# Optimization experiments

Hardware: AMD Instinct MI355X
Metric: run time of the kernel (lower is better)

## Reference

```python
import jax, jax.numpy as jnp
import numpy as np

B, N, IN_FT, OUT_FT = 2, 4096, 512, 256
NEG = -9e15
EPS = 1e-12

def _prelu(x, a):
    return jnp.where(x >= 0, x, a * x)

def _normalize(x):
    n = jnp.sqrt(jnp.sum(x * x, axis=-1, keepdims=True))
    return x / jnp.maximum(n, EPS)

def _xavier(key, shape):
    fan_out, fan_in = shape
    lim = np.sqrt(6.0 / (fan_in + fan_out))
    return jax.random.uniform(key, shape, jnp.float32, -lim, lim)

def setup_inputs() -> dict:
    key = jax.random.key(0)
    ks = jax.random.split(key, 8)
    seq = jax.random.normal(ks[0], (B, N, IN_FT), jnp.float32)
    # sparse-ish random adjacency with self loops, row-normalized (typical GCN input)
    u = jax.random.uniform(ks[1], (B, N, N))
    mask = (u < 0.01).astype(jnp.float32)
    eye = jnp.eye(N, dtype=jnp.float32)[None]
    mask = jnp.maximum(mask, eye)
    adj = mask / jnp.sum(mask, axis=-1, keepdims=True)
    return {
        "seq": seq,
        "adj": adj,
        "W_fc": _xavier(ks[2], (OUT_FT, IN_FT)),
        "W_q": _xavier(ks[3], (OUT_FT, OUT_FT)),
        "W_k": _xavier(ks[4], (OUT_FT, OUT_FT)),
        "W_v1": _xavier(ks[5], (OUT_FT, OUT_FT)),
        "W_v2": _xavier(ks[6], (OUT_FT, OUT_FT)),
        "a_v": jnp.asarray(0.25, jnp.float32),    # PReLU inside to_v
        "a_act": jnp.asarray(0.25, jnp.float32),  # final PReLU self.act
        "bias": jnp.zeros((OUT_FT,), jnp.float32),
    }

def reference(seq, adj, W_fc, W_q, W_k, W_v1, W_v2, a_v, a_act, bias):
    # attn=True, training=False (dropout is identity) path of GCN.forward
    seq_fts = jnp.einsum('bnd,od->bno', seq, W_fc)            # fc (no bias)
    out = jnp.einsum('bmn,bno->bmo', adj, seq_fts)            # bmm(adj, seq_fts)
    out_q = _normalize(jnp.einsum('bno,po->bnp', out, W_q))
    out_k = _normalize(jnp.einsum('bno,po->bnp', out, W_k))
    attn_mx = jax.lax.stop_gradient(jnp.einsum('bmd,bnd->bmn', out_q, out_k))
    div_loss = jnp.mean(jnp.sum((out_q - out_k) ** 2, axis=-1))
    scores = jnp.where(adj > 0, attn_mx, NEG)
    attention = jax.nn.softmax(scores, axis=-1)               # dropout skipped (eval)
    ctx = jnp.einsum('bmn,bno->bmo', attention, out)
    h = _prelu(jnp.einsum('bno,po->bnp', ctx, W_v1), a_v)
    v = jnp.einsum('bno,po->bnp', h, W_v2)
    y = _prelu(v + bias, a_act)
    return (y, div_loss)
```

## Files before the change

kernel.cpp:

```cpp
#include <hip/hip_runtime.h>
#include <hip/hip_bf16.h>


#define NN    4096
#define ROWS  8192
#define OFT   256
#define CAP   128
#define NBLK  512
#define RPB   16
#define EPSN  1e-12f
#define MFMA(a,b,c) __builtin_amdgcn_mfma_f32_16x16x32_bf16((a),(b),(c),0,0,0)

typedef unsigned short ushort_t;
typedef __attribute__((ext_vector_type(8))) short bf16x8;
typedef __attribute__((ext_vector_type(4))) float f32x4;

#define WP_FC   0
#define WP_Q    (16384 * 8)
#define WP_K    (WP_Q + 8192 * 8)
#define WP_V1   (WP_K + 8192 * 8)
#define WP_V2   (WP_V1 + 8192 * 8)

__device__ __forceinline__ float lo_f(unsigned u) { union { unsigned i; float f; } c; c.i = u << 16;          return c.f; }
__device__ __forceinline__ float hi_f(unsigned u) { union { unsigned i; float f; } c; c.i = u & 0xFFFF0000u;  return c.f; }
__device__ __forceinline__ float bf2f(ushort_t u) { union { unsigned i; float f; } c; c.i = (unsigned)u << 16; return c.f; }
__device__ __forceinline__ ushort_t f2bf(float f) {
    union { float f; unsigned i; } c; c.f = f;
    unsigned r = c.i + 0x7FFFu + ((c.i >> 16) & 1u);
    return (ushort_t)(r >> 16);
}
__device__ __forceinline__ unsigned pack2(float a, float b) {
    return (unsigned)f2bf(a) | ((unsigned)f2bf(b) << 16);
}

__device__ __forceinline__ int detect32(const unsigned* w, int tid, int* scnt)
{
    if (tid == 0) *scnt = 0;
    __syncthreads();
    if (tid < 256) {
        union { unsigned i; float f; } c; c.i = w[tid];
        float a = fabsf(c.f);
        if (a > 1e-4f && a < 0.5f) atomicAdd(scnt, 1);
    }
    __syncthreads();
    return *scnt >= 128;
}

__global__ __launch_bounds__(256) void k0_prep(
    const void* __restrict__ Wfc, const void* __restrict__ Wq,
    const void* __restrict__ Wk,  const void* __restrict__ Wv1,
    const void* __restrict__ Wv2, ushort_t* __restrict__ Wp)
{
    __shared__ int scnt;
    const int tid = threadIdx.x;
    const int is32 = detect32((const unsigned*)Wfc, tid, &scnt);
    int sid = blockIdx.x * 256 + tid;
    const void* src; int K, local; ushort_t* dst;
    if (sid < 16384) { src = Wfc; K = 512; local = sid; dst = Wp + WP_FC + (size_t)local * 8; }
    else {
        int s = sid - 16384, which = s >> 13; local = s & 8191;
        const void* ws4[4] = {Wq, Wk, Wv1, Wv2};
        src = ws4[which]; K = 256;
        dst = Wp + WP_Q + (size_t)which * 65536 + (size_t)local * 8;
    }
    int col = local & 255, k8c = local >> 8;
    if (is32) {
        const float* p = (const float*)src + (size_t)col * K + k8c * 8;
        float4 x0 = *(const float4*)p, x1 = *(const float4*)(p + 4);
        uint4 o; o.x = pack2(x0.x, x0.y); o.y = pack2(x0.z, x0.w);
        o.z = pack2(x1.x, x1.y); o.w = pack2(x1.z, x1.w);
        *(uint4*)dst = o;
    } else {
        *(bf16x8*)dst = *(const bf16x8*)((const ushort_t*)src + (size_t)col * K + k8c * 8);
    }
}

__global__ __launch_bounds__(512) void k1_extract_fc(
    const void* __restrict__ seq, const void* __restrict__ adj,
    const void* __restrict__ Wfc, const ushort_t* __restrict__ Wp,
    ushort_t* __restrict__ regA, unsigned* __restrict__ gcv,
    int* __restrict__ cnt)
{
    __shared__ ushort_t Astage[64 * 17 * 8];
    __shared__ unsigned csr_cv[RPB * CAP];
    __shared__ int      csr_n[RPB];
    __shared__ int      scnt;

    const int tid = threadIdx.x, wave = tid >> 6, lane = tid & 63;
    const int t16 = lane & 15, kq = lane >> 4;
    const int b = blockIdx.x, r0 = b * RPB;

    const int is32 = detect32((const unsigned*)Wfc, tid, &scnt);

    for (int rr = 0; rr < 2; ++rr) {
        const int rl = wave * 2 + rr;
        const size_t grow = (size_t)(r0 + rl);
        int cntL = 0, incl, total;
        if (is32) {
            const float4* rowp = (const float4*)((const float*)adj + grow * NN);
            float4 v[16];
#pragma unroll
            for (int t = 0; t < 16; ++t) v[t] = rowp[t * 64 + lane];
#pragma unroll
            for (int t = 0; t < 16; ++t) {
                cntL += (v[t].x > 0.f) + (v[t].y > 0.f) + (v[t].z > 0.f) + (v[t].w > 0.f);
            }
            incl = cntL;
#pragma unroll
            for (int off = 1; off < 64; off <<= 1) {
                int y = __shfl_up(incl, off, 64);
                if (lane >= off) incl += y;
            }
            total = __shfl(incl, 63, 64);
            int p = incl - cntL;
#pragma unroll
            for (int t = 0; t < 16; ++t) {
                float f[4] = {v[t].x, v[t].y, v[t].z, v[t].w};
#pragma unroll
                for (int j = 0; j < 4; ++j)
                    if (f[j] > 0.f) {
                        if (p < CAP) {
                            unsigned col = (t * 64 + lane) * 4 + j;
                            csr_cv[rl * CAP + p] = (col << 16) | f2bf(f[j]);
                        }
                        ++p;
                    }
            }
        } else {
            const uint2* rowp = (const uint2*)((const ushort_t*)adj + grow * NN);
            uint2 v[16];
#pragma unroll
            for (int t = 0; t < 16; ++t) v[t] = rowp[t * 64 + lane];
#pragma unroll
            for (int t = 0; t < 16; ++t) {
                cntL += (lo_f(v[t].x) > 0.f) + (hi_f(v[t].x) > 0.f)
                      + (lo_f(v[t].y) > 0.f) + (hi_f(v[t].y) > 0.f);
            }
            incl = cntL;
#pragma unroll
            for (int off = 1; off < 64; off <<= 1) {
                int y = __shfl_up(incl, off, 64);
                if (lane >= off) incl += y;
            }
            total = __shfl(incl, 63, 64);
            int p = incl - cntL;
#pragma unroll
            for (int t = 0; t < 16; ++t) {
                ushort_t raw[4] = {(ushort_t)(v[t].x & 0xFFFF), (ushort_t)(v[t].x >> 16),
                                   (ushort_t)(v[t].y & 0xFFFF), (ushort_t)(v[t].y >> 16)};
#pragma unroll
                for (int j = 0; j < 4; ++j)
                    if (bf2f(raw[j]) > 0.f) {
                        if (p < CAP) {
                            unsigned col = (t * 64 + lane) * 4 + j;
                            csr_cv[rl * CAP + p] = (col << 16) | raw[j];
                        }
                        ++p;
                    }
            }
        }
        if (lane == 0) csr_n[rl] = (total < CAP) ? total : CAP;
    }
    __syncthreads();
    for (int i = tid; i < RPB * CAP; i += 512)
        gcv[b * (RPB * CAP) + i] = csr_cv[i];
    if (tid < RPB) cnt[r0 + tid] = csr_n[tid];

    {
        int row = tid >> 5, seg = tid & 31;
        bf16x8 f0, f1;
        if (is32) {
            const float* p = (const float*)seq + (size_t)(r0 + row) * 512 + seg * 16;
            float4 x0 = *(const float4*)p, x1 = *(const float4*)(p + 4);
            float4 x2 = *(const float4*)(p + 8), x3 = *(const float4*)(p + 12);
            uint4 a, bq;
            a.x = pack2(x0.x, x0.y); a.y = pack2(x0.z, x0.w);
            a.z = pack2(x1.x, x1.y); a.w = pack2(x1.z, x1.w);
            bq.x = pack2(x2.x, x2.y); bq.y = pack2(x2.z, x2.w);
            bq.z = pack2(x3.x, x3.y); bq.w = pack2(x3.z, x3.w);
            f0 = *(bf16x8*)&a; f1 = *(bf16x8*)&bq;
        } else {
            const ushort_t* p = (const ushort_t*)seq + (size_t)(r0 + row) * 512 + seg * 16;
            f0 = *(const bf16x8*)p; f1 = *(const bf16x8*)(p + 8);
        }
        *(bf16x8*)(Astage + ((seg * 2)     * 17 + row) * 8) = f0;
        *(bf16x8*)(Astage + ((seg * 2 + 1) * 17 + row) * 8) = f1;
    }
    __syncthreads();
    {
        const int col0 = wave * 32 + t16, col1 = col0 + 16;
        const ushort_t* Wm = Wp + WP_FC;
        f32x4 a0 = {0.f,0.f,0.f,0.f}, a1 = {0.f,0.f,0.f,0.f};
        for (int bch = 0; bch < 4; ++bch) {
            bf16x8 wb0[4], wb1[4];
#pragma unroll
            for (int c2 = 0; c2 < 4; ++c2) {
                int k8c = (bch * 4 + c2) * 4 + kq;
                wb0[c2] = *(const bf16x8*)(Wm + ((size_t)k8c * 256 + col0) * 8);
                wb1[c2] = *(const bf16x8*)(Wm + ((size_t)k8c * 256 + col1) * 8);
            }
#pragma unroll
            for (int c2 = 0; c2 < 4; ++c2) {
                int c = bch * 4 + c2;
                bf16x8 af = *(const bf16x8*)(Astage + ((c * 4 + kq) * 17 + t16) * 8);
                a0 = MFMA(af, wb0[c2], a0);
                a1 = MFMA(af, wb1[c2], a1);
            }
        }
#pragma unroll
        for (int r = 0; r < 4; ++r) {
            size_t row = (size_t)(r0 + kq * 4 + r);
            regA[row * OFT + col0] = f2bf(a0[r]);
            regA[row * OFT + col1] = f2bf(a1[r]);
        }
    }
}

__global__ __launch_bounds__(512) void k2_spmm_qk(
    const ushort_t* __restrict__ regA, ushort_t* __restrict__ regC,
    ushort_t* __restrict__ regK, ushort_t* __restrict__ regQ,
    const ushort_t* __restrict__ Wp, const unsigned* __restrict__ gcv,
    const int* __restrict__ cnt, float* __restrict__ part)
{
    __shared__ ushort_t Astage[32 * 17 * 8];
    __shared__ unsigned csr_cv[RPB * CAP];
    __shared__ ushort_t qn_l[RPB * OFT];
    __shared__ float    red[2][RPB][4];
    __shared__ float    dlred[8];

    const int tid = threadIdx.x, wave = tid >> 6, lane = tid & 63;
    const int t16 = lane & 15, kq = lane >> 4;
    const int b = blockIdx.x, r0 = b * RPB;
    const size_t batb = (size_t)(b >> 8) * 4096;

    for (int i = tid; i < RPB * CAP; i += 512)
        csr_cv[i] = gcv[b * (RPB * CAP) + i];
    __syncthreads();

    {
        const int rA = wave * 2, rB = rA + 1;
        const int nA = cnt[r0 + rA], nB = cnt[r0 + rB];
        const int nm = max(nA, nB);
        const ushort_t* gA = regA + batb * OFT;
        float a0[4] = {0,0,0,0}, a1[4] = {0,0,0,0};
        for (int i = 0; i < nm; ++i) {
            if (i < nA) {
                unsigned cv = csr_cv[rA*CAP + i];
                float vvf = bf2f((ushort_t)(cv & 0xFFFF));
                uint2 u = *(const uint2*)(gA + (size_t)(cv >> 16) * OFT + lane * 4);
                a0[0]+=vvf*lo_f(u.x); a0[1]+=vvf*hi_f(u.x); a0[2]+=vvf*lo_f(u.y); a0[3]+=vvf*hi_f(u.y);
            }
            if (i < nB) {
                unsigned cv = csr_cv[rB*CAP + i];
                float vvf = bf2f((ushort_t)(cv & 0xFFFF));
                uint2 u = *(const uint2*)(gA + (size_t)(cv >> 16) * OFT + lane * 4);
                a1[0]+=vvf*lo_f(u.x); a1[1]+=vvf*hi_f(u.x); a1[2]+=vvf*lo_f(u.y); a1[3]+=vvf*hi_f(u.y);
            }
        }
        uint2 s0; s0.x = pack2(a0[0], a0[1]); s0.y = pack2(a0[2], a0[3]);
        uint2 s1; s1.x = pack2(a1[0], a1[1]); s1.y = pack2(a1[2], a1[3]);
        *(uint2*)(regC + (size_t)(r0 + rA) * OFT + lane * 4) = s0;
        *(uint2*)(regC + (size_t)(r0 + rB) * OFT + lane * 4) = s1;
        *(uint2*)(Astage + ((lane >> 1) * 17 + rA) * 8 + (lane & 1) * 4) = s0;
        *(uint2*)(Astage + ((lane >> 1) * 17 + rB) * 8 + (lane & 1) * 4) = s1;
    }
    __syncthreads();

    const int isK = wave >> 2, w4 = wave & 3;
    const ushort_t* Wm = Wp + (isK ? WP_K : WP_Q);
    f32x4 acc[4];
#pragma unroll
    for (int j = 0; j < 4; ++j) acc[j] = (f32x4){0.f,0.f,0.f,0.f};
    for (int bch = 0; bch < 4; ++bch) {
        bf16x8 wb[4][2];
#pragma unroll
        for (int j = 0; j < 4; ++j)
#pragma unroll
            for (int c2 = 0; c2 < 2; ++c2) {
                int col = w4 * 64 + j * 16 + t16;
                int k8c = (bch * 2 + c2) * 4 + kq;
                wb[j][c2] = *(const bf16x8*)(Wm + ((size_t)k8c * 256 + col) * 8);
            }
#pragma unroll
        for (int c2 = 0; c2 < 2; ++c2) {
            int c = bch * 2 + c2;
            bf16x8 af = *(const bf16x8*)(Astage + ((c*4 + kq) * 17 + t16) * 8);
#pragma unroll
            for (int j = 0; j < 4; ++j) acc[j] = MFMA(af, wb[j][c2], acc[j]);
        }
    }
#pragma unroll
    for (int r = 0; r < 4; ++r) {
        float s = 0.f;
#pragma unroll
        for (int j = 0; j < 4; ++j) s += acc[j][r] * acc[j][r];
#pragma unroll
        for (int off = 1; off < 16; off <<= 1) s += __shfl_xor(s, off, 16);
        if (t16 == 0) red[isK][kq*4 + r][w4] = s;
    }
    __syncthreads();
#pragma unroll
    for (int r = 0; r < 4; ++r) {
        int row = kq * 4 + r;
        float s = red[isK][row][0] + red[isK][row][1] + red[isK][row][2] + red[isK][row][3];
        float inv = 1.f / fmaxf(sqrtf(s), EPSN);
#pragma unroll
        for (int j = 0; j < 4; ++j) {
            int col = w4 * 64 + j * 16 + t16;
            float v = acc[j][r] * inv;
            acc[j][r] = v;
            ushort_t uv = f2bf(v);
            if (isK) regK[(size_t)(r0 + row) * OFT + col] = uv;
            else { qn_l[row * OFT + col] = uv; regQ[(size_t)(r0 + row) * OFT + col] = uv; }
        }
    }
    __syncthreads();
    if (isK) {
        float dl = 0.f;
#pragma unroll
        for (int r = 0; r < 4; ++r) {
            int row = kq * 4 + r;
#pragma unroll
            for (int j = 0; j < 4; ++j) {
                int col = w4 * 64 + j * 16 + t16;
                float d = bf2f(qn_l[row * OFT + col]) - acc[j][r];
                dl += d * d;
            }
        }
#pragma unroll
        for (int off = 1; off < 64; off <<= 1) dl += __shfl_xor(dl, off, 64);
        if (lane == 0) dlred[wave] = dl;
    }
    __syncthreads();
    if (tid == 0) part[b] = dlred[4] + dlred[5] + dlred[6] + dlred[7];
}

__global__ __launch_bounds__(512) void k3_attn_v(
    const ushort_t* __restrict__ regC, const ushort_t* __restrict__ regK,
    const ushort_t* __restrict__ regQ, const unsigned* __restrict__ gcv,
    const int* __restrict__ cnt, const ushort_t* __restrict__ Wp,
    const void* __restrict__ Wfc, const void* __restrict__ a_v,
    const void* __restrict__ a_act, const void* __restrict__ biasv,
    const float* __restrict__ part, void* __restrict__ out)
{
    __shared__ ushort_t Astage[32 * 17 * 8];
    __shared__ ushort_t Hl[32 * 17 * 8];
    __shared__ unsigned csr_cv[RPB * CAP];
    __shared__ float    s8[8];
    __shared__ int      scnt;

    const int tid = threadIdx.x, wave = tid >> 6, lane = tid & 63;
    const int t16 = lane & 15, kq = lane >> 4;
    const int b = blockIdx.x, r0 = b * RPB;
    const size_t batb = (size_t)(b >> 8) * 4096;

    const int is32 = detect32((const unsigned*)Wfc, tid, &scnt);

    if (b == 0) {
        float s = part[tid];
#pragma unroll
        for (int off = 32; off; off >>= 1) s += __shfl_down(s, off, 64);
        if (lane == 0) s8[wave] = s;
        __syncthreads();
        if (tid == 0) {
            float t = s8[0]+s8[1]+s8[2]+s8[3]+s8[4]+s8[5]+s8[6]+s8[7];
            float v = t * (1.f / 8192.f);
            if (is32) ((float*)out)[(size_t)ROWS * OFT] = v;
            else      ((ushort_t*)out)[(size_t)ROWS * OFT] = f2bf(v);
        }
    }

    for (int i = tid; i < RPB * CAP; i += 512)
        csr_cv[i] = gcv[b * (RPB * CAP) + i];
    __syncthreads();

    {
        const int rA = wave * 2, rB = rA + 1;
        const int nA = cnt[r0 + rA], nB = cnt[r0 + rB];
        const int nm = max(nA, nB);
        uint2 qa = *(const uint2*)(regQ + (size_t)(r0 + rA) * OFT + lane * 4);
        uint2 qb = *(const uint2*)(regQ + (size_t)(r0 + rB) * OFT + lane * 4);
        float qA[4] = {lo_f(qa.x), hi_f(qa.x), lo_f(qa.y), hi_f(qa.y)};
        float qB[4] = {lo_f(qb.x), hi_f(qb.x), lo_f(qb.y), hi_f(qb.y)};
        const ushort_t* gK = regK + batb * OFT;
        const ushort_t* gO = regC + batb * OFT;
        float sA = 0.f, sB = 0.f;
        float cA[4] = {0,0,0,0}, cB[4] = {0,0,0,0};
        for (int i = 0; i < nm; ++i) {
            if (i < nA) {
                int col = csr_cv[rA*CAP + i] >> 16;
                uint2 kv = *(const uint2*)(gK + (size_t)col * OFT + lane * 4);
                uint2 ov = *(const uint2*)(gO + (size_t)col * OFT + lane * 4);
                float d = lo_f(kv.x)*qA[0] + hi_f(kv.x)*qA[1] + lo_f(kv.y)*qA[2] + hi_f(kv.y)*qA[3];
#pragma unroll
                for (int off = 1; off < 64; off <<= 1) d += __shfl_xor(d, off, 64);
                float es = __expf(d);
                sA += es;
                cA[0]+=es*lo_f(ov.x); cA[1]+=es*hi_f(ov.x); cA[2]+=es*lo_f(ov.y); cA[3]+=es*hi_f(ov.y);
            }
            if (i < nB) {
                int col = csr_cv[rB*CAP + i] >> 16;
                uint2 kv = *(const uint2*)(gK + (size_t)col * OFT + lane * 4);
                uint2 ov = *(const uint2*)(gO + (size_t)col * OFT + lane * 4);
                float d = lo_f(kv.x)*qB[0] + hi_f(kv.x)*qB[1] + lo_f(kv.y)*qB[2] + hi_f(kv.y)*qB[3];
#pragma unroll
                for (int off = 1; off < 64; off <<= 1) d += __shfl_xor(d, off, 64);
                float es = __expf(d);
                sB += es;
                cB[0]+=es*lo_f(ov.x); cB[1]+=es*hi_f(ov.x); cB[2]+=es*lo_f(ov.y); cB[3]+=es*hi_f(ov.y);
            }
        }
        float iA = 1.f / sA, iB = 1.f / sB;
        uint2 s0; s0.x = pack2(cA[0]*iA, cA[1]*iA); s0.y = pack2(cA[2]*iA, cA[3]*iA);
        uint2 s1; s1.x = pack2(cB[0]*iB, cB[1]*iB); s1.y = pack2(cB[2]*iB, cB[3]*iB);
        *(uint2*)(Astage + ((lane >> 1) * 17 + rA) * 8 + (lane & 1) * 4) = s0;
        *(uint2*)(Astage + ((lane >> 1) * 17 + rB) * 8 + (lane & 1) * 4) = s1;
    }
    __syncthreads();

    const int col0 = wave * 32 + t16, col1 = col0 + 16;
    {
        const ushort_t* Wm = Wp + WP_V1;
        f32x4 h0 = {0.f,0.f,0.f,0.f}, h1 = {0.f,0.f,0.f,0.f};
        for (int bch = 0; bch < 2; ++bch) {
            bf16x8 wb0[4], wb1[4];
#pragma unroll
            for (int c2 = 0; c2 < 4; ++c2) {
                int k8c = (bch * 4 + c2) * 4 + kq;
                wb0[c2] = *(const bf16x8*)(Wm + ((size_t)k8c * 256 + col0) * 8);
                wb1[c2] = *(const bf16x8*)(Wm + ((size_t)k8c * 256 + col1) * 8);
            }
#pragma unroll
            for (int c2 = 0; c2 < 4; ++c2) {
                int c = bch * 4 + c2;
                bf16x8 af = *(const bf16x8*)(Astage + ((c*4 + kq) * 17 + t16) * 8);
                h0 = MFMA(af, wb0[c2], h0);
                h1 = MFMA(af, wb1[c2], h1);
            }
        }
        float av = is32 ? *(const float*)a_v : bf2f(*(const ushort_t*)a_v);
        int q0 = col0 >> 3, off0 = col0 & 7, q1 = col1 >> 3;
#pragma unroll
        for (int r = 0; r < 4; ++r) {
            int row = kq * 4 + r;
            float x0 = h0[r]; x0 = (x0 >= 0.f) ? x0 : av * x0;
            float x1 = h1[r]; x1 = (x1 >= 0.f) ? x1 : av * x1;
            Hl[(q0 * 17 + row) * 8 + off0] = f2bf(x0);
            Hl[(q1 * 17 + row) * 8 + off0] = f2bf(x1);
        }
    }
    __syncthreads();

    {
        const ushort_t* Wm = Wp + WP_V2;
        f32x4 y0 = {0.f,0.f,0.f,0.f}, y1 = {0.f,0.f,0.f,0.f};
        for (int bch = 0; bch < 2; ++bch) {
            bf16x8 wb0[4], wb1[4];
#pragma unroll
            for (int c2 = 0; c2 < 4; ++c2) {
                int k8c = (bch * 4 + c2) * 4 + kq;
                wb0[c2] = *(const bf16x8*)(Wm + ((size_t)k8c * 256 + col0) * 8);
                wb1[c2] = *(const bf16x8*)(Wm + ((size_t)k8c * 256 + col1) * 8);
            }
#pragma unroll
            for (int c2 = 0; c2 < 4; ++c2) {
                int c = bch * 4 + c2;
                bf16x8 af = *(const bf16x8*)(Hl + ((c*4 + kq) * 17 + t16) * 8);
                y0 = MFMA(af, wb0[c2], y0);
                y1 = MFMA(af, wb1[c2], y1);
            }
        }
        float aa = is32 ? *(const float*)a_act : bf2f(*(const ushort_t*)a_act);
        float bv0 = is32 ? ((const float*)biasv)[col0] : bf2f(((const ushort_t*)biasv)[col0]);
        float bv1 = is32 ? ((const float*)biasv)[col1] : bf2f(((const ushort_t*)biasv)[col1]);
#pragma unroll
        for (int r = 0; r < 4; ++r) {
            size_t row = (size_t)(r0 + kq * 4 + r);
            float x0 = y0[r] + bv0; x0 = (x0 >= 0.f) ? x0 : aa * x0;
            float x1 = y1[r] + bv1; x1 = (x1 >= 0.f) ? x1 : aa * x1;
            if (is32) {
                ((float*)out)[row * OFT + col0] = x0;
                ((float*)out)[row * OFT + col1] = x1;
            } else {
                ((ushort_t*)out)[row * OFT + col0] = f2bf(x0);
                ((ushort_t*)out)[row * OFT + col1] = f2bf(x1);
            }
        }
    }
}

extern "C" void kernel_launch(void* const* d_in, const int* in_sizes, int n_in,
                              void* d_out, int out_size, void* d_ws, size_t ws_size,
                              hipStream_t stream)
{
    const void* seq   = d_in[0];
    const void* adj   = d_in[1];
    const void* W_fc  = d_in[2];
    const void* W_q   = d_in[3];
    const void* W_k   = d_in[4];
    const void* W_v1  = d_in[5];
    const void* W_v2  = d_in[6];
    const void* a_v   = d_in[7];
    const void* a_act = d_in[8];
    const void* bias  = d_in[9];

    char* w = (char*)d_ws;
    ushort_t* regA = (ushort_t*)w;
    ushort_t* regK = (ushort_t*)(w + (4u  << 20));
    ushort_t* regC = (ushort_t*)(w + (8u  << 20));
    ushort_t* regQ = (ushort_t*)(w + (12u << 20));
    unsigned* gcv  = (unsigned*)(w + (16u << 20));
    int*      cnt  = (int*)(w + (20u << 20));
    float*    part = (float*)(w + (20u << 20) + 32768);
    ushort_t* Wp   = (ushort_t*)(w + (21u << 20));

    k0_prep<<<192, 256, 0, stream>>>(W_fc, W_q, W_k, W_v1, W_v2, Wp);
    k1_extract_fc<<<NBLK, 512, 0, stream>>>(seq, adj, W_fc, Wp, regA, gcv, cnt);
    k2_spmm_qk<<<NBLK, 512, 0, stream>>>(regA, regC, regK, regQ, Wp, gcv, cnt, part);
    k3_attn_v<<<NBLK, 512, 0, stream>>>(regC, regK, regQ, gcv, cnt, Wp,
                                        W_fc, a_v, a_act, bias, part, d_out);
}
```

Measured before the change: 333.9 us.

## Interleave K and context rows, prefetch gathers, widen extract kernel to 1024 threads

The extract/fc kernel now runs 1024 threads with one adjacency row per wave, scanning in four chunks to lower register pressure, and each wave computes a single 16-column MFMA tile. K and the aggregated features are stored interleaved in one buffer, so the attention kernel fetches both with a single 16-byte gather per neighbour instead of two 8-byte gathers. The sparse gather loops in the SpMM and attention kernels software-prefetch the next neighbour's row to hide memory latency. The costs are higher register use from the prefetch and smaller per-wave tiles in the fc GEMM.

```diff
diff --git a/kernel.cpp b/kernel.cpp
--- a/kernel.cpp
+++ b/kernel.cpp
@@ -75,7 +75,7 @@
     }
 }
 
-__global__ __launch_bounds__(512) void k1_extract_fc(
+__global__ __launch_bounds__(1024, 8) void k1_extract_fc(
     const void* __restrict__ seq, const void* __restrict__ adj,
     const void* __restrict__ Wfc, const ushort_t* __restrict__ Wp,
     ushort_t* __restrict__ regA, unsigned* __restrict__ gcv,
@@ -92,135 +92,130 @@
 
     const int is32 = detect32((const unsigned*)Wfc, tid, &scnt);
 
-    for (int rr = 0; rr < 2; ++rr) {
-        const int rl = wave * 2 + rr;
+    {
+        const int rl = wave;
         const size_t grow = (size_t)(r0 + rl);
-        int cntL = 0, incl, total;
+        int base = 0;
         if (is32) {
             const float4* rowp = (const float4*)((const float*)adj + grow * NN);
-            float4 v[16];
-#pragma unroll
-            for (int t = 0; t < 16; ++t) v[t] = rowp[t * 64 + lane];
-#pragma unroll
-            for (int t = 0; t < 16; ++t) {
-                cntL += (v[t].x > 0.f) + (v[t].y > 0.f) + (v[t].z > 0.f) + (v[t].w > 0.f);
-            }
-            incl = cntL;
-#pragma unroll
-            for (int off = 1; off < 64; off <<= 1) {
-                int y = __shfl_up(incl, off, 64);
-                if (lane >= off) incl += y;
-            }
-            total = __shfl(incl, 63, 64);
-            int p = incl - cntL;
-#pragma unroll
-            for (int t = 0; t < 16; ++t) {
-                float f[4] = {v[t].x, v[t].y, v[t].z, v[t].w};
-#pragma unroll
-                for (int j = 0; j < 4; ++j)
-                    if (f[j] > 0.f) {
-                        if (p < CAP) {
-                            unsigned col = (t * 64 + lane) * 4 + j;
-                            csr_cv[rl * CAP + p] = (col << 16) | f2bf(f[j]);
+            for (int h = 0; h < 4; ++h) {
+                float4 v[4];
+#pragma unroll
+                for (int t = 0; t < 4; ++t) v[t] = rowp[(h * 4 + t) * 64 + lane];
+                int c = 0;
+#pragma unroll
+                for (int t = 0; t < 4; ++t)
+                    c += (v[t].x > 0.f) + (v[t].y > 0.f) + (v[t].z > 0.f) + (v[t].w > 0.f);
+                int incl = c;
+#pragma unroll
+                for (int off = 1; off < 64; off <<= 1) {
+                    int y = __shfl_up(incl, off, 64);
+                    if (lane >= off) incl += y;
+                }
+                int p = base + incl - c;
+                base += __shfl(incl, 63, 64);
+#pragma unroll
+                for (int t = 0; t < 4; ++t) {
+                    float f[4] = {v[t].x, v[t].y, v[t].z, v[t].w};
+#pragma unroll
+                    for (int j = 0; j < 4; ++j)
+                        if (f[j] > 0.f) {
+                            if (p < CAP) {
+                                unsigned col = ((h * 4 + t) * 64 + lane) * 4 + j;
+                                csr_cv[rl * CAP + p] = (col << 16) | f2bf(f[j]);
+                            }
+                            ++p;
                         }
-                        ++p;
-                    }
+                }
             }
         } else {
             const uint2* rowp = (const uint2*)((const ushort_t*)adj + grow * NN);
-            uint2 v[16];
-#pragma unroll
-            for (int t = 0; t < 16; ++t) v[t] = rowp[t * 64 + lane];
-#pragma unroll
-            for (int t = 0; t < 16; ++t) {
-                cntL += (lo_f(v[t].x) > 0.f) + (hi_f(v[t].x) > 0.f)
-                      + (lo_f(v[t].y) > 0.f) + (hi_f(v[t].y) > 0.f);
-            }
-            incl = cntL;
-#pragma unroll
-            for (int off = 1; off < 64; off <<= 1) {
-                int y = __shfl_up(incl, off, 64);
-                if (lane >= off) incl += y;
-            }
-            total = __shfl(incl, 63, 64);
-            int p = incl - cntL;
-#pragma unroll
-            for (int t = 0; t < 16; ++t) {
-                ushort_t raw[4] = {(ushort_t)(v[t].x & 0xFFFF), (ushort_t)(v[t].x >> 16),
-                                   (ushort_t)(v[t].y & 0xFFFF), (ushort_t)(v[t].y >> 16)};
-#pragma unroll
-                for (int j = 0; j < 4; ++j)
-                    if (bf2f(raw[j]) > 0.f) {
-                        if (p < CAP) {
-                            unsigned col = (t * 64 + lane) * 4 + j;
-                            csr_cv[rl * CAP + p] = (col << 16) | raw[j];
+            for (int h = 0; h < 4; ++h) {
+                uint2 v[4];
+#pragma unroll
+                for (int t = 0; t < 4; ++t) v[t] = rowp[(h * 4 + t) * 64 + lane];
+                int c = 0;
+#pragma unroll
+                for (int t = 0; t < 4; ++t)
+                    c += (lo_f(v[t].x) > 0.f) + (hi_f(v[t].x) > 0.f)
+                       + (lo_f(v[t].y) > 0.f) + (hi_f(v[t].y) > 0.f);
+                int incl = c;
+#pragma unroll
+                for (int off = 1; off < 64; off <<= 1) {
+                    int y = __shfl_up(incl, off, 64);
+                    if (lane >= off) incl += y;
+                }
+                int p = base + incl - c;
+                base += __shfl(incl, 63, 64);
+#pragma unroll
+                for (int t = 0; t < 4; ++t) {
+                    ushort_t raw[4] = {(ushort_t)(v[t].x & 0xFFFF), (ushort_t)(v[t].x >> 16),
+                                       (ushort_t)(v[t].y & 0xFFFF), (ushort_t)(v[t].y >> 16)};
+#pragma unroll
+                    for (int j = 0; j < 4; ++j)
+                        if (bf2f(raw[j]) > 0.f) {
+                            if (p < CAP) {
+                                unsigned col = ((h * 4 + t) * 64 + lane) * 4 + j;
+                                csr_cv[rl * CAP + p] = (col << 16) | raw[j];
+                            }
+                            ++p;
                         }
-                        ++p;
-                    }
-            }
-        }
-        if (lane == 0) csr_n[rl] = (total < CAP) ? total : CAP;
-    }
-    __syncthreads();
-    for (int i = tid; i < RPB * CAP; i += 512)
+                }
+            }
+        }
+        if (lane == 0) csr_n[rl] = (base < CAP) ? base : CAP;
+    }
+    __syncthreads();
+    for (int i = tid; i < RPB * CAP; i += 1024)
         gcv[b * (RPB * CAP) + i] = csr_cv[i];
     if (tid < RPB) cnt[r0 + tid] = csr_n[tid];
 
     {
-        int row = tid >> 5, seg = tid & 31;
-        bf16x8 f0, f1;
+        int row = tid >> 6, seg = tid & 63;
+        bf16x8 f0;
         if (is32) {
-            const float* p = (const float*)seq + (size_t)(r0 + row) * 512 + seg * 16;
+            const float* p = (const float*)seq + (size_t)(r0 + row) * 512 + seg * 8;
             float4 x0 = *(const float4*)p, x1 = *(const float4*)(p + 4);
-            float4 x2 = *(const float4*)(p + 8), x3 = *(const float4*)(p + 12);
-            uint4 a, bq;
+            uint4 a;
             a.x = pack2(x0.x, x0.y); a.y = pack2(x0.z, x0.w);
             a.z = pack2(x1.x, x1.y); a.w = pack2(x1.z, x1.w);
-            bq.x = pack2(x2.x, x2.y); bq.y = pack2(x2.z, x2.w);
-            bq.z = pack2(x3.x, x3.y); bq.w = pack2(x3.z, x3.w);
-            f0 = *(bf16x8*)&a; f1 = *(bf16x8*)&bq;
+            f0 = *(bf16x8*)&a;
         } else {
-            const ushort_t* p = (const ushort_t*)seq + (size_t)(r0 + row) * 512 + seg * 16;
-            f0 = *(const bf16x8*)p; f1 = *(const bf16x8*)(p + 8);
-        }
-        *(bf16x8*)(Astage + ((seg * 2)     * 17 + row) * 8) = f0;
-        *(bf16x8*)(Astage + ((seg * 2 + 1) * 17 + row) * 8) = f1;
-    }
-    __syncthreads();
-    {
-        const int col0 = wave * 32 + t16, col1 = col0 + 16;
+            f0 = *(const bf16x8*)((const ushort_t*)seq + (size_t)(r0 + row) * 512 + seg * 8);
+        }
+        *(bf16x8*)(Astage + ((size_t)seg * 17 + row) * 8) = f0;
+    }
+    __syncthreads();
+
+    {
+        const int col = wave * 16 + t16;
         const ushort_t* Wm = Wp + WP_FC;
-        f32x4 a0 = {0.f,0.f,0.f,0.f}, a1 = {0.f,0.f,0.f,0.f};
+        f32x4 a0 = {0.f, 0.f, 0.f, 0.f};
         for (int bch = 0; bch < 4; ++bch) {
-            bf16x8 wb0[4], wb1[4];
+            bf16x8 wb[4];
 #pragma unroll
             for (int c2 = 0; c2 < 4; ++c2) {
                 int k8c = (bch * 4 + c2) * 4 + kq;
-                wb0[c2] = *(const bf16x8*)(Wm + ((size_t)k8c * 256 + col0) * 8);
-                wb1[c2] = *(const bf16x8*)(Wm + ((size_t)k8c * 256 + col1) * 8);
+                wb[c2] = *(const bf16x8*)(Wm + ((size_t)k8c * 256 + col) * 8);
             }
 #pragma unroll
             for (int c2 = 0; c2 < 4; ++c2) {
                 int c = bch * 4 + c2;
-                bf16x8 af = *(const bf16x8*)(Astage + ((c * 4 + kq) * 17 + t16) * 8);
-                a0 = MFMA(af, wb0[c2], a0);
-                a1 = MFMA(af, wb1[c2], a1);
-            }
-        }
-#pragma unroll
-        for (int r = 0; r < 4; ++r) {
-            size_t row = (size_t)(r0 + kq * 4 + r);
-            regA[row * OFT + col0] = f2bf(a0[r]);
-            regA[row * OFT + col1] = f2bf(a1[r]);
-        }
+                bf16x8 af = *(const bf16x8*)(Astage + ((size_t)(c * 4 + kq) * 17 + t16) * 8);
+                a0 = MFMA(af, wb[c2], a0);
+            }
+        }
+#pragma unroll
+        for (int r = 0; r < 4; ++r)
+            regA[(size_t)(r0 + kq * 4 + r) * OFT + col] = f2bf(a0[r]);
     }
 }
 
 __global__ __launch_bounds__(512) void k2_spmm_qk(
-    const ushort_t* __restrict__ regA, ushort_t* __restrict__ regC,
-    ushort_t* __restrict__ regK, ushort_t* __restrict__ regQ,
-    const ushort_t* __restrict__ Wp, const unsigned* __restrict__ gcv,
-    const int* __restrict__ cnt, float* __restrict__ part)
+    const ushort_t* __restrict__ regA, ushort_t* __restrict__ regKO,
+    ushort_t* __restrict__ regQ, const ushort_t* __restrict__ Wp,
+    const unsigned* __restrict__ gcv, const int* __restrict__ cnt,
+    float* __restrict__ part)
 {
     __shared__ ushort_t Astage[32 * 17 * 8];
     __shared__ unsigned csr_cv[RPB * CAP];
@@ -243,24 +238,29 @@
         const int nm = max(nA, nB);
         const ushort_t* gA = regA + batb * OFT;
         float a0[4] = {0,0,0,0}, a1[4] = {0,0,0,0};
+        unsigned cvA = 0, cvB = 0;
+        uint2 uA = {0, 0}, uB = {0, 0};
+        if (0 < nA) { cvA = csr_cv[rA*CAP]; uA = *(const uint2*)(gA + (size_t)(cvA >> 16) * OFT + lane * 4); }
+        if (0 < nB) { cvB = csr_cv[rB*CAP]; uB = *(const uint2*)(gA + (size_t)(cvB >> 16) * OFT + lane * 4); }
         for (int i = 0; i < nm; ++i) {
+            unsigned cvA1 = 0, cvB1 = 0;
+            uint2 uA1 = {0, 0}, uB1 = {0, 0};
+            if (i + 1 < nA) { cvA1 = csr_cv[rA*CAP + i + 1]; uA1 = *(const uint2*)(gA + (size_t)(cvA1 >> 16) * OFT + lane * 4); }
+            if (i + 1 < nB) { cvB1 = csr_cv[rB*CAP + i + 1]; uB1 = *(const uint2*)(gA + (size_t)(cvB1 >> 16) * OFT + lane * 4); }
             if (i < nA) {
-                unsigned cv = csr_cv[rA*CAP + i];
-                float vvf = bf2f((ushort_t)(cv & 0xFFFF));
-                uint2 u = *(const uint2*)(gA + (size_t)(cv >> 16) * OFT + lane * 4);
-                a0[0]+=vvf*lo_f(u.x); a0[1]+=vvf*hi_f(u.x); a0[2]+=vvf*lo_f(u.y); a0[3]+=vvf*hi_f(u.y);
+                float vv = bf2f((ushort_t)(cvA & 0xFFFF));
+                a0[0]+=vv*lo_f(uA.x); a0[1]+=vv*hi_f(uA.x); a0[2]+=vv*lo_f(uA.y); a0[3]+=vv*hi_f(uA.y);
             }
             if (i < nB) {
-                unsigned cv = csr_cv[rB*CAP + i];
-                float vvf = bf2f((ushort_t)(cv & 0xFFFF));
-                uint2 u = *(const uint2*)(gA + (size_t)(cv >> 16) * OFT + lane * 4);
-                a1[0]+=vvf*lo_f(u.x); a1[1]+=vvf*hi_f(u.x); a1[2]+=vvf*lo_f(u.y); a1[3]+=vvf*hi_f(u.y);
-            }
+                float vv = bf2f((ushort_t)(cvB & 0xFFFF));
+                a1[0]+=vv*lo_f(uB.x); a1[1]+=vv*hi_f(uB.x); a1[2]+=vv*lo_f(uB.y); a1[3]+=vv*hi_f(uB.y);
+            }
+            cvA = cvA1; uA = uA1; cvB = cvB1; uB = uB1;
         }
         uint2 s0; s0.x = pack2(a0[0], a0[1]); s0.y = pack2(a0[2], a0[3]);
         uint2 s1; s1.x = pack2(a1[0], a1[1]); s1.y = pack2(a1[2], a1[3]);
-        *(uint2*)(regC + (size_t)(r0 + rA) * OFT + lane * 4) = s0;
-        *(uint2*)(regC + (size_t)(r0 + rB) * OFT + lane * 4) = s1;
+        *(uint2*)(regKO + (size_t)(r0 + rA) * 512 + lane * 8 + 4) = s0;
+        *(uint2*)(regKO + (size_t)(r0 + rB) * 512 + lane * 8 + 4) = s1;
         *(uint2*)(Astage + ((lane >> 1) * 17 + rA) * 8 + (lane & 1) * 4) = s0;
         *(uint2*)(Astage + ((lane >> 1) * 17 + rB) * 8 + (lane & 1) * 4) = s1;
     }
@@ -310,7 +310,7 @@
             float v = acc[j][r] * inv;
             acc[j][r] = v;
             ushort_t uv = f2bf(v);
-            if (isK) regK[(size_t)(r0 + row) * OFT + col] = uv;
+            if (isK) regKO[(size_t)(r0 + row) * 512 + (col >> 2) * 8 + (col & 3)] = uv;
             else { qn_l[row * OFT + col] = uv; regQ[(size_t)(r0 + row) * OFT + col] = uv; }
         }
     }
@@ -336,12 +336,12 @@
 }
 
 __global__ __launch_bounds__(512) void k3_attn_v(
-    const ushort_t* __restrict__ regC, const ushort_t* __restrict__ regK,
-    const ushort_t* __restrict__ regQ, const unsigned* __restrict__ gcv,
-    const int* __restrict__ cnt, const ushort_t* __restrict__ Wp,
-    const void* __restrict__ Wfc, const void* __restrict__ a_v,
-    const void* __restrict__ a_act, const void* __restrict__ biasv,
-    const float* __restrict__ part, void* __restrict__ out)
+    const ushort_t* __restrict__ regKO, const ushort_t* __restrict__ regQ,
+    const unsigned* __restrict__ gcv, const int* __restrict__ cnt,
+    const ushort_t* __restrict__ Wp, const void* __restrict__ Wfc,
+    const void* __restrict__ a_v, const void* __restrict__ a_act,
+    const void* __restrict__ biasv, const float* __restrict__ part,
+    void* __restrict__ out)
 {
     __shared__ ushort_t Astage[32 * 17 * 8];
     __shared__ ushort_t Hl[32 * 17 * 8];
@@ -382,33 +382,33 @@
         uint2 qb = *(const uint2*)(regQ + (size_t)(r0 + rB) * OFT + lane * 4);
         float qA[4] = {lo_f(qa.x), hi_f(qa.x), lo_f(qa.y), hi_f(qa.y)};
         float qB[4] = {lo_f(qb.x), hi_f(qb.x), lo_f(qb.y), hi_f(qb.y)};
-        const ushort_t* gK = regK + batb * OFT;
-        const ushort_t* gO = regC + batb * OFT;
+        const ushort_t* gKO = regKO + batb * 512;
         float sA = 0.f, sB = 0.f;
         float cA[4] = {0,0,0,0}, cB[4] = {0,0,0,0};
+        uint4 vA = {0,0,0,0}, vB = {0,0,0,0};
+        if (0 < nA) vA = *(const uint4*)(gKO + (size_t)(csr_cv[rA*CAP] >> 16) * 512 + lane * 8);
+        if (0 < nB) vB = *(const uint4*)(gKO + (size_t)(csr_cv[rB*CAP] >> 16) * 512 + lane * 8);
         for (int i = 0; i < nm; ++i) {
+            uint4 vA1 = {0,0,0,0}, vB1 = {0,0,0,0};
+            if (i + 1 < nA) vA1 = *(const uint4*)(gKO + (size_t)(csr_cv[rA*CAP + i + 1] >> 16) * 512 + lane * 8);
+            if (i + 1 < nB) vB1 = *(const uint4*)(gKO + (size_t)(csr_cv[rB*CAP + i + 1] >> 16) * 512 + lane * 8);
             if (i < nA) {
-                int col = csr_cv[rA*CAP + i] >> 16;
-                uint2 kv = *(const uint2*)(gK + (size_t)col * OFT + lane * 4);
-                uint2 ov = *(const uint2*)(gO + (size_t)col * OFT + lane * 4);
-                float d = lo_f(kv.x)*qA[0] + hi_f(kv.x)*qA[1] + lo_f(kv.y)*qA[2] + hi_f(kv.y)*qA[3];
+                float d = lo_f(vA.x)*qA[0] + hi_f(vA.x)*qA[1] + lo_f(vA.y)*qA[2] + hi_f(vA.y)*qA[3];
 #pragma unroll
                 for (int off = 1; off < 64; off <<= 1) d += __shfl_xor(d, off, 64);
                 float es = __expf(d);
                 sA += es;
-                cA[0]+=es*lo_f(ov.x); cA[1]+=es*hi_f(ov.x); cA[2]+=es*lo_f(ov.y); cA[3]+=es*hi_f(ov.y);
+                cA[0]+=es*lo_f(vA.z); cA[1]+=es*hi_f(vA.z); cA[2]+=es*lo_f(vA.w); cA[3]+=es*hi_f(vA.w);
             }
             if (i < nB) {
-                int col = csr_cv[rB*CAP + i] >> 16;
-                uint2 kv = *(const uint2*)(gK + (size_t)col * OFT + lane * 4);
-                uint2 ov = *(const uint2*)(gO + (size_t)col * OFT + lane * 4);
-                float d = lo_f(kv.x)*qB[0] + hi_f(kv.x)*qB[1] + lo_f(kv.y)*qB[2] + hi_f(kv.y)*qB[3];
+                float d = lo_f(vB.x)*qB[0] + hi_f(vB.x)*qB[1] + lo_f(vB.y)*qB[2] + hi_f(vB.y)*qB[3];
 #pragma unroll
                 for (int off = 1; off < 64; off <<= 1) d += __shfl_xor(d, off, 64);
                 float es = __expf(d);
                 sB += es;
-                cB[0]+=es*lo_f(ov.x); cB[1]+=es*hi_f(ov.x); cB[2]+=es*lo_f(ov.y); cB[3]+=es*hi_f(ov.y);
-            }
+                cB[0]+=es*lo_f(vB.z); cB[1]+=es*hi_f(vB.z); cB[2]+=es*lo_f(vB.w); cB[3]+=es*hi_f(vB.w);
+            }
+            vA = vA1; vB = vB1;
         }
         float iA = 1.f / sA, iB = 1.f / sB;
         uint2 s0; s0.x = pack2(cA[0]*iA, cA[1]*iA); s0.y = pack2(cA[2]*iA, cA[3]*iA);
@@ -505,18 +505,17 @@
     const void* bias  = d_in[9];
 
     char* w = (char*)d_ws;
-    ushort_t* regA = (ushort_t*)w;
-    ushort_t* regK = (ushort_t*)(w + (4u  << 20));
-    ushort_t* regC = (ushort_t*)(w + (8u  << 20));
-    ushort_t* regQ = (ushort_t*)(w + (12u << 20));
-    unsigned* gcv  = (unsigned*)(w + (16u << 20));
-    int*      cnt  = (int*)(w + (20u << 20));
-    float*    part = (float*)(w + (20u << 20) + 32768);
-    ushort_t* Wp   = (ushort_t*)(w + (21u << 20));
+    ushort_t* regA  = (ushort_t*)w;
+    ushort_t* regKO = (ushort_t*)(w + (4u  << 20));
+    ushort_t* regQ  = (ushort_t*)(w + (12u << 20));
+    unsigned* gcv   = (unsigned*)(w + (16u << 20));
+    int*      cnt   = (int*)(w + (20u << 20));
+    float*    part  = (float*)(w + (20u << 20) + 32768);
+    ushort_t* Wp    = (ushort_t*)(w + (21u << 20));
 
     k0_prep<<<192, 256, 0, stream>>>(W_fc, W_q, W_k, W_v1, W_v2, Wp);
-    k1_extract_fc<<<NBLK, 512, 0, stream>>>(seq, adj, W_fc, Wp, regA, gcv, cnt);
-    k2_spmm_qk<<<NBLK, 512, 0, stream>>>(regA, regC, regK, regQ, Wp, gcv, cnt, part);
-    k3_attn_v<<<NBLK, 512, 0, stream>>>(regC, regK, regQ, gcv, cnt, Wp,
+    k1_extract_fc<<<NBLK, 1024, 0, stream>>>(seq, adj, W_fc, Wp, regA, gcv, cnt);
+    k2_spmm_qk<<<NBLK, 512, 0, stream>>>(regA, regKO, regQ, Wp, gcv, cnt, part);
+    k3_attn_v<<<NBLK, 512, 0, stream>>>(regKO, regQ, gcv, cnt, Wp,
                                         W_fc, a_v, a_act, bias, part, d_out);
 }
```

After: 309.9 us. 7.2% less time.
